# Kernel optimization log

Measured on AMD Instinct MI355X. Metric: run time of the kernel, lower is better.

Reference implementation:

```python
import jax, jax.numpy as jnp
import numpy as np

L = 2        # num stacked decoder layers (len(layer_indexes))
S = 2048     # seq_len (prefill)
H = 2048     # hidden_size
NH = 16      # num_heads == num_key_value_heads
D = 128      # head_dim
I = 5632     # intermediate_size
EPS = 1e-6   # rms_norm_eps
NEG = -1e9   # additive causal mask value


def setup_inputs() -> dict:
    key = jax.random.key(0)
    ks = jax.random.split(key, 10)
    scale = 0.02
    hidden_states = jax.random.normal(ks[0], (1, S, H), jnp.float32)
    # causal additive mask, matching the attention_mask parameter in prefill mode
    attention_mask = jnp.where(jnp.tril(jnp.ones((S, S), bool)), 0.0, NEG)[None, None].astype(jnp.float32)
    position_ids = jnp.arange(S, dtype=jnp.int32)[None]
    # Llama rotary tables: (max_seq, head_dim), cos/sin repeated over both halves
    inv_freq = 1.0 / (10000.0 ** (jnp.arange(0, D, 2, dtype=jnp.float32) / D))
    ang = jnp.arange(S, dtype=jnp.float32)[:, None] * inv_freq[None, :]   # [S, D/2]
    cached_cos = jnp.concatenate([jnp.cos(ang), jnp.cos(ang)], axis=-1)   # [S, D]
    cached_sin = jnp.concatenate([jnp.sin(ang), jnp.sin(ang)], axis=-1)
    wq = jax.random.normal(ks[1], (L, H, H), jnp.float32) * scale
    wk = jax.random.normal(ks[2], (L, H, H), jnp.float32) * scale
    wv = jax.random.normal(ks[3], (L, H, H), jnp.float32) * scale
    wo = jax.random.normal(ks[4], (L, H, H), jnp.float32) * scale
    w_gate = jax.random.normal(ks[5], (L, I, H), jnp.float32) * scale
    w_up = jax.random.normal(ks[6], (L, I, H), jnp.float32) * scale
    w_down = jax.random.normal(ks[7], (L, H, I), jnp.float32) * scale
    ln1 = jnp.ones((L, H), jnp.float32)
    ln2 = jnp.ones((L, H), jnp.float32)
    return {"hidden_states": hidden_states, "attention_mask": attention_mask,
            "cached_cos": cached_cos, "cached_sin": cached_sin,
            "wq": wq, "wk": wk, "wv": wv, "wo": wo,
            "w_gate": w_gate, "w_up": w_up, "w_down": w_down,
            "ln1": ln1, "ln2": ln2, "position_ids": position_ids}


def _rms_norm(x, w):
    # variance = mean(x^2) (no mean subtraction), then scale -- exactly as in build_decoder
    var = jnp.mean(x * x, axis=-1, keepdims=True)
    return (x / jnp.sqrt(var + EPS)) * w


def _rotate_half(x):
    x1, x2 = jnp.split(x, 2, axis=-1)
    return jnp.concatenate([-x2, x1], axis=-1)


def _rope(x, cos, sin):
    return x * cos + _rotate_half(x) * sin


def _forward(hidden_states, attention_mask, cached_cos, cached_sin,
             wq, wk, wv, wo, w_gate, w_up, w_down, ln1, ln2, position_ids):
    pos = position_ids[0]                              # [S]
    cos = cached_cos[pos][None, None]                  # [1,1,S,D]
    sin = cached_sin[pos][None, None]
    inv_sqrt_d = 1.0 / np.sqrt(D).astype(np.float32)
    x = hidden_states                                  # [1,S,H]
    for i in range(L):
        h = _rms_norm(x, ln1[i])
        q = (h @ wq[i].T).reshape(1, S, NH, D).transpose(0, 2, 1, 3)  # [1,NH,S,D]
        k = (h @ wk[i].T).reshape(1, S, NH, D).transpose(0, 2, 1, 3)
        v = (h @ wv[i].T).reshape(1, S, NH, D).transpose(0, 2, 1, 3)
        q = _rope(q, cos, sin)
        k = _rope(k, cos, sin)
        scores = jnp.einsum('bhqd,bhkd->bhqk', q, k) * inv_sqrt_d + attention_mask
        attn = jax.nn.softmax(scores, axis=-1)
        o = jnp.einsum('bhqk,bhkd->bhqd', attn, v)
        o = o.transpose(0, 2, 1, 3).reshape(1, S, H)
        x = x + o @ wo[i].T
        h = _rms_norm(x, ln2[i])
        mlp = (jax.nn.silu(h @ w_gate[i].T) * (h @ w_up[i].T)) @ w_down[i].T
        x = x + mlp
    return x


def reference(hidden_states, attention_mask, cached_cos, cached_sin,
              wq, wk, wv, wo, w_gate, w_up, w_down, ln1, ln2, position_ids):
    return _forward(hidden_states, attention_mask, cached_cos, cached_sin,
                    wq, wk, wv, wo, w_gate, w_up, w_down, ln1, ln2, position_ids)
```

## Files before the change

kernel.cpp:

```cpp
#include <hip/hip_runtime.h>
#include <hip/hip_bf16.h>

constexpr int kL = 2;
constexpr int kS = 2048;
constexpr int kH = 2048;
constexpr int kNH = 16;
constexpr int kD = 128;
constexpr int kI = 5632;

using s16x8 = __attribute__((ext_vector_type(8))) short;
using s16x4 = __attribute__((ext_vector_type(4))) short;
using f32x4 = __attribute__((ext_vector_type(4))) float;

__device__ __forceinline__ float b2f(short s) {
  union { unsigned u; float f; } v;
  v.u = ((unsigned)(unsigned short)s) << 16;
  return v.f;
}
__device__ __forceinline__ short f2bs(float f) {
  __hip_bfloat16 h = __float2bfloat16(f);
  union { __hip_bfloat16 h; short s; } u;
  u.h = h;
  return u.s;
}

__device__ __forceinline__ void lds16(const void* g, void* l) {
  __builtin_amdgcn_global_load_lds(
      (const __attribute__((address_space(1))) void*)g,
      (__attribute__((address_space(3))) void*)l, 16, 0, 0);
}

__device__ __forceinline__ void swz_block(int gx, int& bx, int& by) {
  const int gy = gridDim.y;
  const int lin = by * gx + bx;
  if ((gx & 3) == 0 && (gy & 1) == 0) {
    const int cx = gx >> 2, cy = gy >> 1;
    const int xcd = lin & 7;
    const int s = lin >> 3;
    bx = (xcd & 3) * cx + s / cy;
    by = (xcd >> 2) * cy + s % cy;
  } else if (((gx * gy) & 7) == 0) {
    const int cpx = (gx * gy) >> 3;
    const int l2 = (lin & 7) * cpx + (lin >> 3);
    bx = l2 % gx;
    by = l2 / gx;
  }
}

__global__ __launch_bounds__(256) void cvt_all(const float* __restrict__ q,
                                               const float* __restrict__ k,
                                               const float* __restrict__ v,
                                               const float* __restrict__ o,
                                               const float* __restrict__ g,
                                               const float* __restrict__ u,
                                               const float* __restrict__ d,
                                               short* __restrict__ dst) {
  constexpr int HH8 = (kH * kH) / 8;
  constexpr int IH8 = (kI * kH) / 8;
  constexpr int tot = 4 * HH8 + 3 * IH8;
  for (int i = blockIdx.x * blockDim.x + threadIdx.x; i < tot; i += gridDim.x * blockDim.x) {
    const float* src;
    int off;
    if (i < 4 * HH8) {
      const int s = i >> 19;
      off = i & (HH8 - 1);
      src = s == 0 ? q : s == 1 ? k : s == 2 ? v : o;
    } else {
      const int j = i - 4 * HH8;
      const int s = j / IH8;
      off = j - s * IH8;
      src = s == 0 ? g : s == 1 ? u : d;
    }
    const float4 a = ((const float4*)src)[2 * off];
    const float4 b = ((const float4*)src)[2 * off + 1];
    s16x8 ov;
    ov[0] = f2bs(a.x); ov[1] = f2bs(a.y); ov[2] = f2bs(a.z); ov[3] = f2bs(a.w);
    ov[4] = f2bs(b.x); ov[5] = f2bs(b.y); ov[6] = f2bs(b.z); ov[7] = f2bs(b.w);
    ((s16x8*)dst)[i] = ov;
  }
}

template <int EPI>
__global__ __launch_bounds__(256) void gemm_db(const short* __restrict__ A,
                                               const short* __restrict__ B,
                                               short* __restrict__ C0,
                                               short* __restrict__ C1,
                                               short* __restrict__ C2,
                                               float* __restrict__ Cf,
                                               int M, int N, int K) {
  __shared__ short As0[128 * 64], Bs0[128 * 64];
  __shared__ short As1[128 * 64], Bs1[128 * 64];
  const int t = threadIdx.x;
  const int lane = t & 63, wid = t >> 6;
  int bx = blockIdx.x, by = blockIdx.y;
  swz_block(gridDim.x, bx, by);
  const int m0 = by * 128, n0 = bx * 128;
  const int wr = (wid >> 1) * 64, wc = (wid & 1) * 64;
  const int fr = lane & 15, g4 = lane >> 4;

  const int srow = (lane >> 3);
  const int scol = (((lane & 7) << 4) ^ (srow << 4)) >> 1;

  f32x4 acc[4][4] = {};

  auto stage = [&](short* Ad, short* Bd, int k0) {
    #pragma unroll
    for (int c = 0; c < 4; ++c) {
      const int chunk = wid * 4 + c;
      const int e0 = chunk * 512;
      const int row = chunk * 8 + srow;
      lds16(A + (size_t)(m0 + row) * K + k0 + scol, Ad + e0);
      lds16(B + (size_t)(n0 + row) * K + k0 + scol, Bd + e0);
    }
  };

  auto compute = [&](const short* Xs, const short* Ys) {
    #pragma unroll
    for (int ks = 0; ks < 2; ++ks) {
      s16x8 a[4], b[4];
      #pragma unroll
      for (int m = 0; m < 4; ++m) {
        const int r = wr + m * 16 + fr;
        a[m] = *(const s16x8*)&Xs[r * 64 + (((ks * 4 + g4) ^ (r & 7)) << 3)];
      }
      #pragma unroll
      for (int n = 0; n < 4; ++n) {
        const int r = wc + n * 16 + fr;
        b[n] = *(const s16x8*)&Ys[r * 64 + (((ks * 4 + g4) ^ (r & 7)) << 3)];
      }
      #pragma unroll
      for (int m = 0; m < 4; ++m)
        #pragma unroll
        for (int n = 0; n < 4; ++n)
          acc[m][n] = __builtin_amdgcn_mfma_f32_16x16x32_bf16(a[m], b[n], acc[m][n], 0, 0, 0);
    }
  };

  const int nt = K >> 6;
  stage(As0, Bs0, 0);
  __syncthreads();
  for (int tt = 0; tt < nt; tt += 2) {
    stage(As1, Bs1, (tt + 1) << 6);
    compute(As0, Bs0);
    __syncthreads();
    if (tt + 2 < nt) stage(As0, Bs0, (tt + 2) << 6);
    compute(As1, Bs1);
    __syncthreads();
  }

  #pragma unroll
  for (int m = 0; m < 4; ++m) {
    #pragma unroll
    for (int n = 0; n < 4; ++n) {
      const int rb = m0 + wr + m * 16 + g4 * 4;
      const int col = n0 + wc + n * 16 + fr;
      if (EPI == 1) {
        #pragma unroll
        for (int j = 0; j < 4; ++j)
          Cf[(size_t)(rb + j) * N + col] += acc[m][n][j];
      } else if (EPI == 3) {
        const int seg = n0 >> 11;
        const int cl = col - (seg << 11);
        if (seg == 0) {
          #pragma unroll
          for (int j = 0; j < 4; ++j) C0[(size_t)(rb + j) * 2048 + cl] = f2bs(acc[m][n][j]);
        } else if (seg == 1) {
          #pragma unroll
          for (int j = 0; j < 4; ++j) C1[(size_t)(rb + j) * 2048 + cl] = f2bs(acc[m][n][j]);
        } else {
          s16x4 pk;
          #pragma unroll
          for (int j = 0; j < 4; ++j) pk[j] = f2bs(acc[m][n][j]);
          *(s16x4*)&C2[(size_t)cl * M + rb] = pk;
        }
      } else {
        const bool useg = (n0 >= 5632);
        const int cl = col - (useg ? 5632 : 0);
        short* dst = useg ? C1 : C0;
        #pragma unroll
        for (int j = 0; j < 4; ++j) dst[(size_t)(rb + j) * 5632 + cl] = f2bs(acc[m][n][j]);
      }
    }
  }
}

template <int EPI>
__global__ __launch_bounds__(256) void gemm_btf(const short* __restrict__ A,
                                                const float* __restrict__ B,
                                                short* __restrict__ Cb,
                                                float* __restrict__ Cf,
                                                int M, int N, int K) {
  __shared__ short As[128 * 32];
  __shared__ short Bs[128 * 32];
  const int t = threadIdx.x;
  const int lane = t & 63, wid = t >> 6;
  int bx = blockIdx.x, by = blockIdx.y;
  swz_block(gridDim.x, bx, by);
  const int m0 = by * 128, n0 = bx * 128;
  const int wr = (wid >> 1) * 64, wc = (wid & 1) * 64;
  const int fr = lane & 15, h8 = (lane >> 4) * 8;
  const int brow = t >> 1, bcol = (t & 1) * 16;
  const float* bsrc = B + (size_t)(n0 + brow) * K + bcol;

  f32x4 acc[4][4] = {};

  for (int k0 = 0; k0 < K; k0 += 32) {
    const float4 bv0 = *(const float4*)(bsrc + k0);
    const float4 bv1 = *(const float4*)(bsrc + k0 + 4);
    const float4 bv2 = *(const float4*)(bsrc + k0 + 8);
    const float4 bv3 = *(const float4*)(bsrc + k0 + 12);
    __syncthreads();
    {
      const float bf[16] = {bv0.x, bv0.y, bv0.z, bv0.w, bv1.x, bv1.y, bv1.z, bv1.w,
                            bv2.x, bv2.y, bv2.z, bv2.w, bv3.x, bv3.y, bv3.z, bv3.w};
      s16x8 wlo, whi;
      #pragma unroll
      for (int j = 0; j < 8; ++j) { wlo[j] = f2bs(bf[j]); whi[j] = f2bs(bf[8 + j]); }
      *(s16x8*)&Bs[brow * 32 + bcol] = wlo;
      *(s16x8*)&Bs[brow * 32 + bcol + 8] = whi;
    }
    #pragma unroll
    for (int c = 0; c < 2; ++c) {
      const int e0 = c * 2048 + wid * 512;
      const int e = e0 + lane * 8;
      const int row = e >> 5, col = e & 31;
      lds16(A + (size_t)(m0 + row) * K + k0 + col, (void*)(As + e0));
    }
    __syncthreads();

    s16x8 a[4], b[4];
    #pragma unroll
    for (int m = 0; m < 4; ++m) a[m] = *(const s16x8*)&As[(wr + m * 16 + fr) * 32 + h8];
    #pragma unroll
    for (int n = 0; n < 4; ++n) b[n] = *(const s16x8*)&Bs[(wc + n * 16 + fr) * 32 + h8];
    #pragma unroll
    for (int m = 0; m < 4; ++m)
      #pragma unroll
      for (int n = 0; n < 4; ++n)
        acc[m][n] = __builtin_amdgcn_mfma_f32_16x16x32_bf16(a[m], b[n], acc[m][n], 0, 0, 0);
  }

  const int g4 = lane >> 4;
  #pragma unroll
  for (int m = 0; m < 4; ++m) {
    #pragma unroll
    for (int n = 0; n < 4; ++n) {
      const int rb = m0 + wr + m * 16 + g4 * 4;
      const int col = n0 + wc + n * 16 + fr;
      if (EPI == 0) {
        #pragma unroll
        for (int j = 0; j < 4; ++j)
          Cb[(size_t)(rb + j) * N + col] = f2bs(acc[m][n][j]);
      } else if (EPI == 1) {
        #pragma unroll
        for (int j = 0; j < 4; ++j)
          Cf[(size_t)(rb + j) * N + col] += acc[m][n][j];
      } else {
        s16x4 pk;
        #pragma unroll
        for (int j = 0; j < 4; ++j) pk[j] = f2bs(acc[m][n][j]);
        *(s16x4*)&Cb[(size_t)col * M + rb] = pk;
      }
    }
  }
}

__global__ __launch_bounds__(256) void rmsnorm_k(const float* __restrict__ x,
                                                 const float* __restrict__ w,
                                                 short* __restrict__ h) {
  const int row = blockIdx.x, t = threadIdx.x;
  const float4* xr = (const float4*)(x + (size_t)row * kH);
  const float4 v0 = xr[2 * t], v1 = xr[2 * t + 1];
  float ss = v0.x * v0.x + v0.y * v0.y + v0.z * v0.z + v0.w * v0.w +
             v1.x * v1.x + v1.y * v1.y + v1.z * v1.z + v1.w * v1.w;
  #pragma unroll
  for (int off = 1; off < 64; off <<= 1) ss += __shfl_xor(ss, off);
  __shared__ float red[4];
  if ((t & 63) == 0) red[t >> 6] = ss;
  __syncthreads();
  ss = red[0] + red[1] + red[2] + red[3];
  const float rs = rsqrtf(ss * (1.0f / kH) + 1e-6f);
  const float4 w0 = ((const float4*)w)[2 * t];
  const float4 w1 = ((const float4*)w)[2 * t + 1];
  const float xv[8] = {v0.x, v0.y, v0.z, v0.w, v1.x, v1.y, v1.z, v1.w};
  const float wv[8] = {w0.x, w0.y, w0.z, w0.w, w1.x, w1.y, w1.z, w1.w};
  s16x8 o;
  #pragma unroll
  for (int j = 0; j < 8; ++j) o[j] = f2bs(xv[j] * rs * wv[j]);
  *(s16x8*)&h[(size_t)row * kH + t * 8] = o;
}

__global__ __launch_bounds__(256) void rope_k(short* __restrict__ q, short* __restrict__ k,
                                              const float* __restrict__ cosb,
                                              const float* __restrict__ sinb,
                                              const int* __restrict__ pos) {
  const int s = blockIdx.x;
  const int p = pos[s];
  const size_t rowb = (size_t)s * kH;
  for (int idx = threadIdx.x; idx < kNH * 64; idx += 256) {
    const int hh = idx >> 6, d = idx & 63;
    const float c = cosb[p * kD + d];
    const float sn = sinb[p * kD + d];
    const size_t i1 = rowb + hh * kD + d, i2 = i1 + 64;
    const float q1 = b2f(q[i1]), q2 = b2f(q[i2]);
    q[i1] = f2bs(q1 * c - q2 * sn);
    q[i2] = f2bs(q2 * c + q1 * sn);
    const float k1 = b2f(k[i1]), k2 = b2f(k[i2]);
    k[i1] = f2bs(k1 * c - k2 * sn);
    k[i2] = f2bs(k2 * c + k1 * sn);
  }
}

__global__ __launch_bounds__(256) void attn_k(const short* __restrict__ q,
                                              const short* __restrict__ k,
                                              const short* __restrict__ vt,
                                              short* __restrict__ o) {
  __shared__ short Kl[2][64 * 128];
  __shared__ short Vl[2][128 * 64];
  __shared__ short Pl[4][16 * 72];
  const int h = blockIdx.x;
  const int qi = blockIdx.y;
  const int t = threadIdx.x;
  const int lane = t & 63, wid = t >> 6;
  const int fr = lane & 15, g4 = lane >> 4;
  const int q0 = qi * 64 + wid * 16;

  s16x8 aq[4];
  {
    const short* qp = q + (size_t)(q0 + fr) * kH + h * kD;
    #pragma unroll
    for (int ks = 0; ks < 4; ++ks) aq[ks] = *(const s16x8*)(qp + ks * 32 + g4 * 8);
  }
  f32x4 acco[8] = {};
  float mrun[4], lrun[4];
  #pragma unroll
  for (int j = 0; j < 4; ++j) { mrun[j] = -3.0e30f; lrun[j] = 0.f; }

  s16x8 kreg[4], vreg[4];
  auto loadt = [&](int tt) {
    const int kv0 = tt * 64;
    #pragma unroll
    for (int c = 0; c < 4; ++c) {
      const int b = c * 4096 + t * 16;
      kreg[c] = *(const s16x8*)(k + (size_t)(kv0 + (b >> 8)) * kH + h * kD + ((b & 255) >> 1));
      vreg[c] = *(const s16x8*)(vt + (size_t)(h * kD + (b >> 7)) * kS + kv0 + ((b & 127) >> 1));
    }
  };
  auto writet = [&](int buf) {
    #pragma unroll
    for (int c = 0; c < 4; ++c) {
      const int b = c * 4096 + t * 16;
      const int kr = b >> 8, kc = b & 255;
      *(s16x8*)((char*)Kl[buf] + kr * 256 + (kc ^ ((kr & 7) << 4))) = kreg[c];
      const int vr = b >> 7, vc = b & 127;
      *(s16x8*)((char*)Vl[buf] + vr * 128 + (vc ^ ((vr & 7) << 4))) = vreg[c];
    }
  };

  loadt(0);
  writet(0);
  __syncthreads();

  for (int tt = 0; tt <= qi; ++tt) {
    const int kv0 = tt * 64;
    const int cur = tt & 1;
    if (tt < qi) loadt(tt + 1);

    f32x4 sc[4] = {};
    __builtin_amdgcn_s_setprio(1);
    #pragma unroll
    for (int ks = 0; ks < 4; ++ks) {
      const int ch16 = ks * 4 + g4;
      #pragma unroll
      for (int nf = 0; nf < 4; ++nf) {
        const int row = nf * 16 + fr;
        const s16x8 bk =
            *(const s16x8*)((const char*)Kl[cur] + row * 256 + ((ch16 ^ (row & 7)) << 4));
        sc[nf] = __builtin_amdgcn_mfma_f32_16x16x32_bf16(aq[ks], bk, sc[nf], 0, 0, 0);
      }
    }
    __builtin_amdgcn_s_setprio(0);

    float val[4][4];
    #pragma unroll
    for (int nf = 0; nf < 4; ++nf) {
      #pragma unroll
      for (int j = 0; j < 4; ++j) {
        float v = sc[nf][j] * 0.08838834764831845f;
        if (tt == qi) {
          const int colg = kv0 + nf * 16 + fr;
          const int rowg = q0 + g4 * 4 + j;
          if (colg > rowg) v -= 1.0e9f;
        }
        val[nf][j] = v;
      }
    }

    #pragma unroll
    for (int j = 0; j < 4; ++j) {
      float rm = fmaxf(fmaxf(val[0][j], val[1][j]), fmaxf(val[2][j], val[3][j]));
      rm = fmaxf(rm, __shfl_xor(rm, 1));
      rm = fmaxf(rm, __shfl_xor(rm, 2));
      rm = fmaxf(rm, __shfl_xor(rm, 4));
      rm = fmaxf(rm, __shfl_xor(rm, 8));
      const float mnew = fmaxf(mrun[j], rm);
      const float corr = __expf(mrun[j] - mnew);
      mrun[j] = mnew;
      float ps = 0.f;
      #pragma unroll
      for (int nf = 0; nf < 4; ++nf) {
        const float p = __expf(val[nf][j] - mnew);
        ps += p;
        Pl[wid][(g4 * 4 + j) * 72 + nf * 16 + fr] = f2bs(p);
      }
      ps += __shfl_xor(ps, 1);
      ps += __shfl_xor(ps, 2);
      ps += __shfl_xor(ps, 4);
      ps += __shfl_xor(ps, 8);
      lrun[j] = lrun[j] * corr + ps;
      #pragma unroll
      for (int nf = 0; nf < 8; ++nf) acco[nf][j] *= corr;
    }

    __builtin_amdgcn_s_setprio(1);
    #pragma unroll
    for (int ks = 0; ks < 2; ++ks) {
      const s16x8 ap = *(const s16x8*)(&Pl[wid][fr * 72 + ks * 32 + g4 * 8]);
      const int ch16 = ks * 4 + g4;
      #pragma unroll
      for (int nf = 0; nf < 8; ++nf) {
        const int dd = nf * 16 + fr;
        const s16x8 bv =
            *(const s16x8*)((const char*)Vl[cur] + dd * 128 + ((ch16 ^ (dd & 7)) << 4));
        acco[nf] = __builtin_amdgcn_mfma_f32_16x16x32_bf16(ap, bv, acco[nf], 0, 0, 0);
      }
    }
    __builtin_amdgcn_s_setprio(0);

    if (tt < qi) writet(cur ^ 1);
    __syncthreads();
  }

  #pragma unroll
  for (int nf = 0; nf < 8; ++nf) {
    #pragma unroll
    for (int j = 0; j < 4; ++j) {
      const int rowg = q0 + g4 * 4 + j;
      o[(size_t)rowg * kH + h * kD + nf * 16 + fr] = f2bs(acco[nf][j] / lrun[j]);
    }
  }
}

__global__ void silu_mul(short* __restrict__ g, const short* __restrict__ u, int n8) {
  for (int i = blockIdx.x * blockDim.x + threadIdx.x; i < n8; i += gridDim.x * blockDim.x) {
    const s16x8 gv = ((const s16x8*)g)[i];
    const s16x8 uv = ((const s16x8*)u)[i];
    s16x8 o;
    #pragma unroll
    for (int j = 0; j < 8; ++j) {
      const float gf = b2f(gv[j]);
      const float s = gf / (1.f + __expf(-gf));
      o[j] = f2bs(s * b2f(uv[j]));
    }
    ((s16x8*)g)[i] = o;
  }
}

extern "C" void kernel_launch(void* const* d_in, const int* in_sizes, int n_in,
                              void* d_out, int out_size, void* d_ws, size_t ws_size,
                              hipStream_t stream) {
  (void)in_sizes; (void)n_in; (void)out_size;
  const float* hidden = (const float*)d_in[0];
  const float* cosb = (const float*)d_in[2];
  const float* sinb = (const float*)d_in[3];
  const float* wq = (const float*)d_in[4];
  const float* wk = (const float*)d_in[5];
  const float* wv = (const float*)d_in[6];
  const float* wo = (const float*)d_in[7];
  const float* wg = (const float*)d_in[8];
  const float* wu = (const float*)d_in[9];
  const float* wd = (const float*)d_in[10];
  const float* ln1 = (const float*)d_in[11];
  const float* ln2 = (const float*)d_in[12];
  const int* pos = (const int*)d_in[13];
  float* out = (float*)d_out;

  char* p = (char*)d_ws;
  float* x  = (float*)p;  p += (size_t)kS * kH * 4;
  short* hb = (short*)p;  p += (size_t)kS * kH * 2;
  char* U = p;            p += (size_t)kS * kI * 4;
  short* qb = (short*)(U);
  short* kb = (short*)(U + (size_t)kS * kH * 2);
  short* vtb = (short*)(U + (size_t)kS * kH * 4);
  short* ob = (short*)(U + (size_t)kS * kH * 6);
  short* gb = (short*)(U);
  short* ub = (short*)(U + (size_t)kS * kI * 2);
  short* wbuf = (short*)p;
  const size_t nHH = (size_t)kH * kH, nIH = (size_t)kI * kH;
  const size_t need = (size_t)(p - (char*)d_ws) + (4 * nHH + 3 * nIH) * 2;
  const bool pre = ws_size >= need;

  short* wqb = wbuf;
  short* wob = wqb + 3 * nHH;
  short* wgb = wob + nHH;
  short* wdb = wgb + 2 * nIH;

  hipMemcpyAsync(x, hidden, (size_t)kS * kH * 4, hipMemcpyDeviceToDevice, stream);
  for (int l = 0; l < kL; ++l) {
    rmsnorm_k<<<kS, 256, 0, stream>>>(x, ln1 + (size_t)l * kH, hb);
    if (pre) {
      cvt_all<<<2048, 256, 0, stream>>>(wq + l * nHH, wk + l * nHH, wv + l * nHH,
                                        wo + l * nHH, wg + l * nIH, wu + l * nIH,
                                        wd + l * nIH, wbuf);
      gemm_db<3><<<dim3(6144 / 128, kS / 128), 256, 0, stream>>>(
          hb, wqb, qb, kb, vtb, nullptr, kS, 6144, kH);
      rope_k<<<kS, 256, 0, stream>>>(qb, kb, cosb, sinb, pos);
      attn_k<<<dim3(kNH, kS / 64), 256, 0, stream>>>(qb, kb, vtb, ob);
      gemm_db<1><<<dim3(kH / 128, kS / 128), 256, 0, stream>>>(
          ob, wob, nullptr, nullptr, nullptr, x, kS, kH, kH);
      rmsnorm_k<<<kS, 256, 0, stream>>>(x, ln2 + (size_t)l * kH, hb);
      gemm_db<4><<<dim3(11264 / 128, kS / 128), 256, 0, stream>>>(
          hb, wgb, gb, ub, nullptr, nullptr, kS, 11264, kH);
      silu_mul<<<1408, 256, 0, stream>>>(gb, ub, kS * kI / 8);
      gemm_db<1><<<dim3(kH / 128, kS / 128), 256, 0, stream>>>(
          gb, wdb, nullptr, nullptr, nullptr, x, kS, kH, kI);
    } else {
      gemm_btf<0><<<dim3(kH / 128, kS / 128), 256, 0, stream>>>(hb, wq + l * nHH, qb, nullptr, kS, kH, kH);
      gemm_btf<0><<<dim3(kH / 128, kS / 128), 256, 0, stream>>>(hb, wk + l * nHH, kb, nullptr, kS, kH, kH);
      gemm_btf<2><<<dim3(kH / 128, kS / 128), 256, 0, stream>>>(hb, wv + l * nHH, vtb, nullptr, kS, kH, kH);
      rope_k<<<kS, 256, 0, stream>>>(qb, kb, cosb, sinb, pos);
      attn_k<<<dim3(kNH, kS / 64), 256, 0, stream>>>(qb, kb, vtb, ob);
      gemm_btf<1><<<dim3(kH / 128, kS / 128), 256, 0, stream>>>(ob, wo + l * nHH, nullptr, x, kS, kH, kH);
      rmsnorm_k<<<kS, 256, 0, stream>>>(x, ln2 + (size_t)l * kH, hb);
      gemm_btf<0><<<dim3(kI / 128, kS / 128), 256, 0, stream>>>(hb, wg + l * nIH, gb, nullptr, kS, kI, kH);
      gemm_btf<0><<<dim3(kI / 128, kS / 128), 256, 0, stream>>>(hb, wu + l * nIH, ub, nullptr, kS, kI, kH);
      silu_mul<<<1408, 256, 0, stream>>>(gb, ub, kS * kI / 8);
      gemm_btf<1><<<dim3(kH / 128, kS / 128), 256, 0, stream>>>(gb, wd + l * nIH, nullptr, x, kS, kH, kI);
    }
  }
  hipMemcpyAsync(out, x, (size_t)kS * kH * 4, hipMemcpyDeviceToDevice, stream);
}
```

Measured before the change: 956.2 us.

## Use 256x256-tile triple-buffered GEMM for QKV and gate/up projections

Adds a new GEMM kernel with 256x256 output tiles, 512 threads (8 waves), a 3-stage LDS ring of K=32 slices with explicit vmcnt waits, and raised wave priority around the MFMA block. The fused QKV and gate/up projections now use it, while the fp32-accumulating output and down projections keep the old 128x128 double-buffered kernel. The larger tiles cut global reads per FLOP, and deeper prefetch hides load latency. The cost is higher register pressure from 32 accumulators per lane and fewer blocks (192 and 352), which may leave some CUs idle or unbalanced.

```diff
diff --git a/kernel.cpp b/kernel.cpp
--- a/kernel.cpp
+++ b/kernel.cpp
@@ -81,84 +81,90 @@
 }
 
 template <int EPI>
-__global__ __launch_bounds__(256) void gemm_db(const short* __restrict__ A,
-                                               const short* __restrict__ B,
-                                               short* __restrict__ C0,
-                                               short* __restrict__ C1,
-                                               short* __restrict__ C2,
-                                               float* __restrict__ Cf,
-                                               int M, int N, int K) {
-  __shared__ short As0[128 * 64], Bs0[128 * 64];
-  __shared__ short As1[128 * 64], Bs1[128 * 64];
+__global__ __launch_bounds__(512, 2) void gemm256t(const short* __restrict__ A,
+                                                   const short* __restrict__ B,
+                                                   short* __restrict__ C0,
+                                                   short* __restrict__ C1,
+                                                   short* __restrict__ C2,
+                                                   int M, int N, int K) {
+  __shared__ short AsAll[3 * 256 * 32];
+  __shared__ short BsAll[3 * 256 * 32];
   const int t = threadIdx.x;
   const int lane = t & 63, wid = t >> 6;
   int bx = blockIdx.x, by = blockIdx.y;
   swz_block(gridDim.x, bx, by);
-  const int m0 = by * 128, n0 = bx * 128;
-  const int wr = (wid >> 1) * 64, wc = (wid & 1) * 64;
+  const int m0 = by * 256, n0 = bx * 256;
+  const int wr = (wid >> 2) * 128, wc = (wid & 3) * 64;
   const int fr = lane & 15, g4 = lane >> 4;
 
-  const int srow = (lane >> 3);
-  const int scol = (((lane & 7) << 4) ^ (srow << 4)) >> 1;
-
-  f32x4 acc[4][4] = {};
-
-  auto stage = [&](short* Ad, short* Bd, int k0) {
-    #pragma unroll
-    for (int c = 0; c < 4; ++c) {
-      const int chunk = wid * 4 + c;
-      const int e0 = chunk * 512;
-      const int row = chunk * 8 + srow;
-      lds16(A + (size_t)(m0 + row) * K + k0 + scol, Ad + e0);
-      lds16(B + (size_t)(n0 + row) * K + k0 + scol, Bd + e0);
+  const int srow = lane >> 2;
+  const int scol = ((lane & 3) ^ ((lane >> 3) & 3)) << 3;
+
+  f32x4 acc[8][4] = {};
+
+  auto stageT = [&](int tt, int buf) {
+    const int k0 = tt << 5;
+    short* Ad = AsAll + buf * 8192;
+    short* Bd = BsAll + buf * 8192;
+    #pragma unroll
+    for (int c2 = 0; c2 < 2; ++c2) {
+      const int c = wid * 2 + c2;
+      lds16(A + (size_t)(m0 + c * 16 + srow) * K + k0 + scol, Ad + c * 512);
+      lds16(B + (size_t)(n0 + c * 16 + srow) * K + k0 + scol, Bd + c * 512);
     }
   };
 
-  auto compute = [&](const short* Xs, const short* Ys) {
-    #pragma unroll
-    for (int ks = 0; ks < 2; ++ks) {
-      s16x8 a[4], b[4];
-      #pragma unroll
-      for (int m = 0; m < 4; ++m) {
-        const int r = wr + m * 16 + fr;
-        a[m] = *(const s16x8*)&Xs[r * 64 + (((ks * 4 + g4) ^ (r & 7)) << 3)];
-      }
-      #pragma unroll
-      for (int n = 0; n < 4; ++n) {
-        const int r = wc + n * 16 + fr;
-        b[n] = *(const s16x8*)&Ys[r * 64 + (((ks * 4 + g4) ^ (r & 7)) << 3)];
-      }
-      #pragma unroll
-      for (int m = 0; m < 4; ++m)
-        #pragma unroll
-        for (int n = 0; n < 4; ++n)
-          acc[m][n] = __builtin_amdgcn_mfma_f32_16x16x32_bf16(a[m], b[n], acc[m][n], 0, 0, 0);
-    }
+  auto computeT = [&](int buf) {
+    const short* Xs = AsAll + buf * 8192;
+    const short* Ys = BsAll + buf * 8192;
+    s16x8 a[8], b[4];
+    #pragma unroll
+    for (int m = 0; m < 8; ++m) {
+      const int r = wr + m * 16 + fr;
+      a[m] = *(const s16x8*)&Xs[r * 32 + ((g4 ^ ((r >> 1) & 3)) << 3)];
+    }
+    #pragma unroll
+    for (int n = 0; n < 4; ++n) {
+      const int r = wc + n * 16 + fr;
+      b[n] = *(const s16x8*)&Ys[r * 32 + ((g4 ^ ((r >> 1) & 3)) << 3)];
+    }
+    __builtin_amdgcn_s_setprio(1);
+    #pragma unroll
+    for (int m = 0; m < 8; ++m)
+      #pragma unroll
+      for (int n = 0; n < 4; ++n)
+        acc[m][n] = __builtin_amdgcn_mfma_f32_16x16x32_bf16(a[m], b[n], acc[m][n], 0, 0, 0);
+    __builtin_amdgcn_s_setprio(0);
   };
 
-  const int nt = K >> 6;
-  stage(As0, Bs0, 0);
-  __syncthreads();
-  for (int tt = 0; tt < nt; tt += 2) {
-    stage(As1, Bs1, (tt + 1) << 6);
-    compute(As0, Bs0);
-    __syncthreads();
-    if (tt + 2 < nt) stage(As0, Bs0, (tt + 2) << 6);
-    compute(As1, Bs1);
-    __syncthreads();
+  const int nt = K >> 5;
+  stageT(0, 0);
+  stageT(1, 1);
+  asm volatile("s_waitcnt vmcnt(4)" ::: "memory");
+  __builtin_amdgcn_s_barrier();
+  int cur = 0, nx = 2;
+  for (int tt = 0; tt < nt; ++tt) {
+    if (tt + 2 < nt) stageT(tt + 2, nx);
+    computeT(cur);
+    if (tt + 1 < nt) {
+      if (tt + 2 < nt) {
+        asm volatile("s_waitcnt vmcnt(4)" ::: "memory");
+      } else {
+        asm volatile("s_waitcnt vmcnt(0)" ::: "memory");
+      }
+      __builtin_amdgcn_s_barrier();
+    }
+    cur = cur + 1; if (cur == 3) cur = 0;
+    nx = nx + 1; if (nx == 3) nx = 0;
   }
 
   #pragma unroll
-  for (int m = 0; m < 4; ++m) {
+  for (int m = 0; m < 8; ++m) {
     #pragma unroll
     for (int n = 0; n < 4; ++n) {
       const int rb = m0 + wr + m * 16 + g4 * 4;
       const int col = n0 + wc + n * 16 + fr;
-      if (EPI == 1) {
-        #pragma unroll
-        for (int j = 0; j < 4; ++j)
-          Cf[(size_t)(rb + j) * N + col] += acc[m][n][j];
-      } else if (EPI == 3) {
+      if (EPI == 3) {
         const int seg = n0 >> 11;
         const int cl = col - (seg << 11);
         if (seg == 0) {
@@ -182,6 +188,88 @@
       }
     }
   }
+}
+
+template <int EPI>
+__global__ __launch_bounds__(256) void gemm_db(const short* __restrict__ A,
+                                               const short* __restrict__ B,
+                                               short* __restrict__ C0,
+                                               short* __restrict__ C1,
+                                               short* __restrict__ C2,
+                                               float* __restrict__ Cf,
+                                               int M, int N, int K) {
+  __shared__ short As0[128 * 64], Bs0[128 * 64];
+  __shared__ short As1[128 * 64], Bs1[128 * 64];
+  const int t = threadIdx.x;
+  const int lane = t & 63, wid = t >> 6;
+  int bx = blockIdx.x, by = blockIdx.y;
+  swz_block(gridDim.x, bx, by);
+  const int m0 = by * 128, n0 = bx * 128;
+  const int wr = (wid >> 1) * 64, wc = (wid & 1) * 64;
+  const int fr = lane & 15, g4 = lane >> 4;
+
+  const int srow = (lane >> 3);
+  const int scol = (((lane & 7) << 4) ^ (srow << 4)) >> 1;
+
+  f32x4 acc[4][4] = {};
+
+  auto stage = [&](short* Ad, short* Bd, int k0) {
+    #pragma unroll
+    for (int c = 0; c < 4; ++c) {
+      const int chunk = wid * 4 + c;
+      const int e0 = chunk * 512;
+      const int row = chunk * 8 + srow;
+      lds16(A + (size_t)(m0 + row) * K + k0 + scol, Ad + e0);
+      lds16(B + (size_t)(n0 + row) * K + k0 + scol, Bd + e0);
+    }
+  };
+
+  auto compute = [&](const short* Xs, const short* Ys) {
+    #pragma unroll
+    for (int ks = 0; ks < 2; ++ks) {
+      s16x8 a[4], b[4];
+      #pragma unroll
+      for (int m = 0; m < 4; ++m) {
+        const int r = wr + m * 16 + fr;
+        a[m] = *(const s16x8*)&Xs[r * 64 + (((ks * 4 + g4) ^ (r & 7)) << 3)];
+      }
+      #pragma unroll
+      for (int n = 0; n < 4; ++n) {
+        const int r = wc + n * 16 + fr;
+        b[n] = *(const s16x8*)&Ys[r * 64 + (((ks * 4 + g4) ^ (r & 7)) << 3)];
+      }
+      #pragma unroll
+      for (int m = 0; m < 4; ++m)
+        #pragma unroll
+        for (int n = 0; n < 4; ++n)
+          acc[m][n] = __builtin_amdgcn_mfma_f32_16x16x32_bf16(a[m], b[n], acc[m][n], 0, 0, 0);
+    }
+  };
+
+  const int nt = K >> 6;
+  stage(As0, Bs0, 0);
+  __syncthreads();
+  for (int tt = 0; tt < nt; tt += 2) {
+    stage(As1, Bs1, (tt + 1) << 6);
+    compute(As0, Bs0);
+    __syncthreads();
+    if (tt + 2 < nt) stage(As0, Bs0, (tt + 2) << 6);
+    compute(As1, Bs1);
+    __syncthreads();
+  }
+
+  #pragma unroll
+  for (int m = 0; m < 4; ++m) {
+    #pragma unroll
+    for (int n = 0; n < 4; ++n) {
+      const int rb = m0 + wr + m * 16 + g4 * 4;
+      const int col = n0 + wc + n * 16 + fr;
+      #pragma unroll
+      for (int j = 0; j < 4; ++j)
+        Cf[(size_t)(rb + j) * N + col] += acc[m][n][j];
+    }
+  }
+  (void)C0; (void)C1; (void)C2;
 }
 
 template <int EPI>
@@ -512,15 +600,15 @@
       cvt_all<<<2048, 256, 0, stream>>>(wq + l * nHH, wk + l * nHH, wv + l * nHH,
                                         wo + l * nHH, wg + l * nIH, wu + l * nIH,
                                         wd + l * nIH, wbuf);
-      gemm_db<3><<<dim3(6144 / 128, kS / 128), 256, 0, stream>>>(
-          hb, wqb, qb, kb, vtb, nullptr, kS, 6144, kH);
+      gemm256t<3><<<dim3(6144 / 256, kS / 256), 512, 0, stream>>>(
+          hb, wqb, qb, kb, vtb, kS, 6144, kH);
       rope_k<<<kS, 256, 0, stream>>>(qb, kb, cosb, sinb, pos);
       attn_k<<<dim3(kNH, kS / 64), 256, 0, stream>>>(qb, kb, vtb, ob);
       gemm_db<1><<<dim3(kH / 128, kS / 128), 256, 0, stream>>>(
           ob, wob, nullptr, nullptr, nullptr, x, kS, kH, kH);
       rmsnorm_k<<<kS, 256, 0, stream>>>(x, ln2 + (size_t)l * kH, hb);
-      gemm_db<4><<<dim3(11264 / 128, kS / 128), 256, 0, stream>>>(
-          hb, wgb, gb, ub, nullptr, nullptr, kS, 11264, kH);
+      gemm256t<4><<<dim3(11264 / 256, kS / 256), 512, 0, stream>>>(
+          hb, wgb, gb, ub, nullptr, kS, 11264, kH);
       silu_mul<<<1408, 256, 0, stream>>>(gb, ub, kS * kI / 8);
       gemm_db<1><<<dim3(kH / 128, kS / 128), 256, 0, stream>>>(
           gb, wdb, nullptr, nullptr, nullptr, x, kS, kH, kI);
```

Result: slower. 1.078 ms (+12.7%).
